# Kernel optimization log

Measured on AMD Instinct MI355X. Metric: run time of the kernel, lower is better.

Reference implementation:

```python
import jax, jax.numpy as jnp
import numpy as np

TOP_K = 4
N_GROUP = 8
TOPK_GROUP = 4
SCALE = 1.0

B, S, H, I, E = 2, 1024, 1024, 512, 32
SHARED_I = I * 2  # n_shared_experts = 2


def setup_inputs() -> dict:
    key = jax.random.key(0)
    ks = jax.random.split(key, 9)
    return {
        "hidden_states": jax.random.normal(ks[0], (B, S, H), jnp.float32),
        "gate_w": jax.random.normal(ks[1], (E, H), jnp.float32) * 0.02,
        "gate_bias": jnp.zeros((E,), jnp.float32),
        "gate_proj": jax.random.normal(ks[2], (E, I, H), jnp.float32) * 0.02,
        "up_proj": jax.random.normal(ks[3], (E, I, H), jnp.float32) * 0.02,
        "down_proj": jax.random.normal(ks[4], (E, H, I), jnp.float32) * 0.02,
        "shared_gate_w": jax.random.normal(ks[5], (SHARED_I, H), jnp.float32) * 0.02,
        "shared_up_w": jax.random.normal(ks[6], (SHARED_I, H), jnp.float32) * 0.02,
        "shared_down_w": jax.random.normal(ks[7], (H, SHARED_I), jnp.float32) * 0.02,
    }


def reference(hidden_states, gate_w, gate_bias, gate_proj, up_proj, down_proj,
              shared_gate_w, shared_up_w, shared_down_w):
    b, s, h = hidden_states.shape
    e = gate_w.shape[0]
    x = hidden_states.reshape(-1, h)            # (T, H)
    t = x.shape[0]

    # ---- gating (DeepSeek-V3 grouped sigmoid routing) ----
    logits = x @ gate_w.T                       # (T, E)
    scores = jax.nn.sigmoid(logits)
    sfc = scores + gate_bias[None, :]           # scores_for_choice
    # per-group score = sum of top-2 experts in group
    group_scores = jax.lax.top_k(sfc.reshape(t, N_GROUP, -1), 2)[0].sum(-1)  # (T, G)
    _, gidx = jax.lax.top_k(group_scores, TOPK_GROUP)                        # (T, topk_group)
    gmask = jax.nn.one_hot(gidx, N_GROUP, dtype=sfc.dtype).sum(1)            # (T, G)
    smask = jnp.repeat(gmask, e // N_GROUP, axis=1)                          # (T, E)
    tmp = jnp.where(smask > 0, sfc, 0.0)
    _, topk_idx = jax.lax.top_k(tmp, TOP_K)                                  # (T, K)
    topk_w = jnp.take_along_axis(scores, topk_idx, axis=1)                   # (T, K)
    topk_w = topk_w / (topk_w.sum(-1, keepdims=True) + 1e-20)                # norm_topk_prob
    topk_w = topk_w * SCALE

    # ---- routed experts (dense combine-weight formulation) ----
    comb = jnp.zeros((t, e), x.dtype).at[jnp.arange(t)[:, None], topk_idx].add(topk_w)  # (T, E)
    g = jnp.einsum('th,eih->eti', x, gate_proj)   # (E, T, I)
    u = jnp.einsum('th,eih->eti', x, up_proj)     # (E, T, I)
    a = jax.nn.silu(g) * u
    a = a * comb.T[:, :, None]                    # scale before down-proj to skip zero experts
    out = jnp.einsum('eti,ehi->th', a, down_proj) # (T, H)

    # ---- shared experts ----
    sg = x @ shared_gate_w.T
    su = x @ shared_up_w.T
    out = out + (jax.nn.silu(sg) * su) @ shared_down_w.T

    return out.reshape(b, s, h)
```

## Files before the change

kernel.cpp:

```cpp
#include <hip/hip_runtime.h>
#include <hip/hip_bf16.h>
#include <cstdint>
#include <cstddef>

#define H_DIM 1024
#define I_DIM 512
#define E_NUM 32
#define SHARED_I_DIM 1024
#define TOPK 4
#define NGROUP 8
#define TOPKG 4
#define GT 8

typedef __attribute__((ext_vector_type(8))) short bf16x8;
typedef __attribute__((ext_vector_type(4))) float f32x4;
typedef __attribute__((ext_vector_type(8))) unsigned short u16x8;

__device__ inline unsigned short f2bf(float f) {
    __hip_bfloat16 h = __float2bfloat16(f);
    return *reinterpret_cast<unsigned short*>(&h);
}
__device__ inline float bf2f(unsigned short u) {
    union { unsigned int u; float f; } w;
    w.u = ((unsigned int)u) << 16;
    return w.f;
}

__device__ inline int laddr(int row, int chunk) {
    return row * 32 + ((chunk ^ ((row >> 1) & 3)) << 3);
}

__global__ void init_kernel(int* cnt) {
    if (threadIdx.x < 64) cnt[threadIdx.x] = 0;
}

__global__ void cvt_kernel(const float* __restrict__ src, unsigned short* __restrict__ dst, int n8) {
    int i = blockIdx.x * blockDim.x + threadIdx.x;
    if (i >= n8) return;
    float4 a = *(const float4*)(src + (size_t)i * 8);
    float4 b = *(const float4*)(src + (size_t)i * 8 + 4);
    u16x8 v;
    v[0] = f2bf(a.x); v[1] = f2bf(a.y); v[2] = f2bf(a.z); v[3] = f2bf(a.w);
    v[4] = f2bf(b.x); v[5] = f2bf(b.y); v[6] = f2bf(b.z); v[7] = f2bf(b.w);
    *(u16x8*)(dst + (size_t)i * 8) = v;
}

__global__ __launch_bounds__(256) void gate_kernel(const float* __restrict__ x,
                                                   const float* __restrict__ gw,
                                                   float* __restrict__ logits_out) {
    int tb = blockIdx.x;
    int tid = threadIdx.x;
    __shared__ float xs[GT][H_DIM];
    __shared__ float ps[8][GT][E_NUM];
    const float* xsrc = x + (size_t)tb * GT * H_DIM;
    for (int i = tid; i < GT * H_DIM / 4; i += 256)
        ((float4*)&xs[0][0])[i] = ((const float4*)xsrc)[i];
    __syncthreads();
    int e = tid & 31, part = tid >> 5;
    const float* wrow = gw + (size_t)e * H_DIM + part * 128;
    float acc[GT] = {};
    for (int c0 = 0; c0 < 128; c0 += 32) {
        float w[32];
#pragma unroll
        for (int c = 0; c < 32; c++) w[c] = wrow[c0 + c];
#pragma unroll
        for (int t = 0; t < GT; t++) {
#pragma unroll
            for (int c = 0; c < 32; c++)
                acc[t] += w[c] * xs[t][part * 128 + c0 + c];
        }
    }
#pragma unroll
    for (int t = 0; t < GT; t++) ps[part][t][e] = acc[t];
    __syncthreads();
    {
        int t = tid >> 5, ee = tid & 31;
        float s = 0.f;
#pragma unroll
        for (int p = 0; p < 8; p++) s += ps[p][t][ee];
        logits_out[((size_t)tb * GT + t) * E_NUM + ee] = s;
    }
}

__global__ void select_kernel(const float* __restrict__ logits, const float* __restrict__ gb,
                              int* __restrict__ topk_e, float* __restrict__ topk_w,
                              int* __restrict__ cnt, int T) {
    int t = blockIdx.x * blockDim.x + threadIdx.x;
    if (t >= T) return;
    float scores[E_NUM], sfc[E_NUM];
#pragma unroll
    for (int i = 0; i < E_NUM; i++) {
        float l = logits[(size_t)t * E_NUM + i];
        float s = 1.f / (1.f + expf(-l));
        scores[i] = s;
        sfc[i] = s + gb[i];
    }
    float gs[NGROUP];
#pragma unroll
    for (int g = 0; g < NGROUP; g++) {
        float m1 = -1e30f, m2 = -1e30f;
#pragma unroll
        for (int j = 0; j < 4; j++) {
            float v = sfc[g * 4 + j];
            if (v > m1) { m2 = m1; m1 = v; }
            else if (v > m2) { m2 = v; }
        }
        gs[g] = m1 + m2;
    }
    unsigned gmask = 0;
    for (int r = 0; r < TOPKG; r++) {
        int best = 0; float bv = -1e30f;
#pragma unroll
        for (int g = 0; g < NGROUP; g++)
            if (!((gmask >> g) & 1u) && gs[g] > bv) { bv = gs[g]; best = g; }
        gmask |= 1u << best;
    }
    unsigned cmask = 0;
    int eidx[TOPK]; float ew[TOPK]; float sum = 0.f;
    for (int r = 0; r < TOPK; r++) {
        int best = 0; float bv = -1e30f; float bsc = 0.f;
#pragma unroll
        for (int i = 0; i < E_NUM; i++) {
            float v = ((gmask >> (i >> 2)) & 1u) ? sfc[i] : 0.0f;
            if (!((cmask >> i) & 1u) && v > bv) { bv = v; best = i; bsc = scores[i]; }
        }
        cmask |= 1u << best;
        eidx[r] = best; ew[r] = bsc; sum += bsc;
    }
    float inv = 1.f / (sum + 1e-20f);
#pragma unroll
    for (int k = 0; k < TOPK; k++) {
        topk_e[t * TOPK + k] = eidx[k];
        topk_w[t * TOPK + k] = ew[k] * inv;
        atomicAdd(&cnt[eidx[k]], 1);
    }
}

__global__ void scan_kernel(const int* __restrict__ cnt, int* __restrict__ off) {
    if (threadIdx.x == 0) {
        int a = 0;
        for (int e = 0; e < E_NUM; e++) { off[e] = a; a += cnt[e]; }
        off[E_NUM] = a;
    }
}

__global__ void bin_kernel(const int* __restrict__ topk_e, const float* __restrict__ topk_w,
                           const int* __restrict__ off, int* __restrict__ cnt2,
                           int* __restrict__ slot_token, float* __restrict__ slot_w,
                           int* __restrict__ slot_of, int total) {
    int i = blockIdx.x * blockDim.x + threadIdx.x;
    if (i >= total) return;
    int e = topk_e[i];
    float w = topk_w[i];
    int pos = atomicAdd(&cnt2[e], 1);
    int slot = off[e] + pos;
    slot_token[slot] = i >> 2;
    slot_w[slot] = w;
    slot_of[i] = slot;
}

__global__ __launch_bounds__(256) void combine_kernel(const unsigned short* __restrict__ out_slot,
                                                      const int* __restrict__ slot_of,
                                                      float* __restrict__ out) {
    int t = blockIdx.x;
    int h = threadIdx.x * 4;
    int s0 = slot_of[t * TOPK + 0], s1 = slot_of[t * TOPK + 1];
    int s2 = slot_of[t * TOPK + 2], s3 = slot_of[t * TOPK + 3];
    ushort4 a = *(const ushort4*)(out_slot + (size_t)s0 * H_DIM + h);
    ushort4 b = *(const ushort4*)(out_slot + (size_t)s1 * H_DIM + h);
    ushort4 c = *(const ushort4*)(out_slot + (size_t)s2 * H_DIM + h);
    ushort4 d = *(const ushort4*)(out_slot + (size_t)s3 * H_DIM + h);
    float4 o = *(float4*)(out + (size_t)t * H_DIM + h);
    o.x += bf2f(a.x) + bf2f(b.x) + bf2f(c.x) + bf2f(d.x);
    o.y += bf2f(a.y) + bf2f(b.y) + bf2f(c.y) + bf2f(d.y);
    o.z += bf2f(a.z) + bf2f(b.z) + bf2f(c.z) + bf2f(d.z);
    o.w += bf2f(a.w) + bf2f(b.w) + bf2f(c.w) + bf2f(d.w);
    *(float4*)(out + (size_t)t * H_DIM + h) = o;
}

template <bool STAGE1>
__global__ __launch_bounds__(512, 2) void moe_gemm(
    const unsigned short* __restrict__ Axr, const unsigned short* __restrict__ Axs,
    const float* __restrict__ B1r_, const float* __restrict__ B2r_,
    const float* __restrict__ B1s_, const float* __restrict__ B2s_,
    void* __restrict__ Dr, void* __restrict__ Ds,
    const int* __restrict__ slot_token, const float* __restrict__ slot_w,
    const int* __restrict__ cnt, const int* __restrict__ off_arr, int T) {
    constexpr bool DUAL = STAGE1;
    int e = blockIdx.x, itile = blockIdx.y, mtile = blockIdx.z;
    bool sh = (e == E_NUM);
    int NI = STAGE1 ? (sh ? 16 : 8) : 16;
    if (itile >= NI) return;
    int count = sh ? T : cnt[e];
    int base = sh ? 0 : off_arr[e];
    if (mtile * 256 >= count) return;
    const int K = STAGE1 ? H_DIM : (sh ? SHARED_I_DIM : I_DIM);

    __shared__ __align__(16) unsigned short As[2][256 * 32];
    __shared__ __align__(16) unsigned short Bs1[2][64 * 32];
    __shared__ __align__(16) unsigned short Bs2[2][DUAL ? 64 * 32 : 8];

    int tid = threadIdx.x, lane = tid & 63, wid = tid >> 6;

    int as_row = tid >> 1, as_c0 = (tid & 1) * 2;
    int am = mtile * 256 + as_row;
    int amc = (am < count) ? am : 0;
    const unsigned short* Abase;
    size_t arow;
    if constexpr (STAGE1) {
        Abase = Axr;
        arow = sh ? (size_t)amc : (size_t)slot_token[base + amc];
    } else {
        Abase = sh ? Axs : Axr;
        arow = sh ? (size_t)amc : (size_t)(base + amc);
    }
    const unsigned short* Ga = Abase + arow * K + as_c0 * 8;

    int bs_row = tid >> 3;
    int brow = itile * 64 + bs_row;
    int bwr = laddr(bs_row, (tid & 7) >> 1) + (tid & 1) * 4;
    const float* Gb1;
    const float* Gb2 = nullptr;
    if constexpr (STAGE1) {
        Gb1 = (sh ? B1s_ : (B1r_ + (size_t)e * (I_DIM * H_DIM))) + (size_t)brow * K + (tid & 7) * 4;
        Gb2 = (sh ? B2s_ : (B2r_ + (size_t)e * (I_DIM * H_DIM))) + (size_t)brow * K + (tid & 7) * 4;
    } else {
        Gb1 = (sh ? B1s_ : (B1r_ + (size_t)e * (H_DIM * I_DIM))) + (size_t)brow * K + (tid & 7) * 4;
    }

    f32x4 acc1[4][2] = {};
    f32x4 acc2[DUAL ? 4 : 1][2] = {};

    int wrow = (wid >> 1) * 64, wcol = (wid & 1) * 32;
    int frow = lane & 15, fch = lane >> 4;

    u16x8 a00, a01, a10, a11;
    float4 b10, b20, b11, b21;

    auto loadS = [&](u16x8& a0, u16x8& a1, float4& b1v, float4& b2v, int ks) {
        int k0 = ks << 5;
        a0 = *(const u16x8*)(Ga + k0);
        a1 = *(const u16x8*)(Ga + k0 + 8);
        b1v = *(const float4*)(Gb1 + k0);
        if constexpr (DUAL) b2v = *(const float4*)(Gb2 + k0);
    };
    auto writeS = [&](int buf, u16x8 a0, u16x8 a1, float4 b1v, float4 b2v) {
        *(u16x8*)(&As[buf][laddr(as_row, as_c0)]) = a0;
        *(u16x8*)(&As[buf][laddr(as_row, as_c0 + 1)]) = a1;
        ushort4 s;
        s.x = f2bf(b1v.x); s.y = f2bf(b1v.y); s.z = f2bf(b1v.z); s.w = f2bf(b1v.w);
        *(ushort4*)(&Bs1[buf][bwr]) = s;
        if constexpr (DUAL) {
            ushort4 s2;
            s2.x = f2bf(b2v.x); s2.y = f2bf(b2v.y); s2.z = f2bf(b2v.z); s2.w = f2bf(b2v.w);
            *(ushort4*)(&Bs2[buf][bwr]) = s2;
        }
    };
    auto compute = [&](int buf) {
        bf16x8 af[4], b1[2], b2[DUAL ? 2 : 1];
#pragma unroll
        for (int nf = 0; nf < 2; nf++)
            b1[nf] = *(const bf16x8*)(&Bs1[buf][laddr(wcol + nf * 16 + frow, fch)]);
        if constexpr (DUAL) {
#pragma unroll
            for (int nf = 0; nf < 2; nf++)
                b2[nf] = *(const bf16x8*)(&Bs2[buf][laddr(wcol + nf * 16 + frow, fch)]);
        }
#pragma unroll
        for (int mf = 0; mf < 4; mf++)
            af[mf] = *(const bf16x8*)(&As[buf][laddr(wrow + mf * 16 + frow, fch)]);
#pragma unroll
        for (int mf = 0; mf < 4; mf++)
#pragma unroll
            for (int nf = 0; nf < 2; nf++) {
                acc1[mf][nf] = __builtin_amdgcn_mfma_f32_16x16x32_bf16(af[mf], b1[nf], acc1[mf][nf], 0, 0, 0);
                if constexpr (DUAL)
                    acc2[mf][nf] = __builtin_amdgcn_mfma_f32_16x16x32_bf16(af[mf], b2[nf], acc2[mf][nf], 0, 0, 0);
            }
    };

    const int NK = K >> 5;
    loadS(a00, a01, b10, b20, 0);
    loadS(a10, a11, b11, b21, 1);
    writeS(0, a00, a01, b10, b20);
    loadS(a00, a01, b10, b20, 2);
    __syncthreads();
    for (int it = 0; it < NK; it += 2) {
        writeS(1, a10, a11, b11, b21);
        if (it + 3 < NK) loadS(a10, a11, b11, b21, it + 3);
        compute(0);
        __syncthreads();
        if (it + 2 < NK) {
            writeS(0, a00, a01, b10, b20);
            if (it + 4 < NK) loadS(a00, a01, b10, b20, it + 4);
        }
        compute(1);
        if (it + 2 < NK) __syncthreads();
    }

#pragma unroll
    for (int mf = 0; mf < 4; mf++)
#pragma unroll
        for (int nf = 0; nf < 2; nf++)
#pragma unroll
            for (int j = 0; j < 4; j++) {
                int rloc = wrow + mf * 16 + (lane >> 4) * 4 + j;
                int mrow = mtile * 256 + rloc;
                int col = itile * 64 + wcol + nf * 16 + (lane & 15);
                if (mrow >= count) continue;
                if constexpr (STAGE1) {
                    float w = sh ? 1.0f : slot_w[base + mrow];
                    float g = acc1[mf][nf][j];
                    float a = (g / (1.f + __expf(-g))) * acc2[mf][nf][j] * w;
                    if (sh) ((unsigned short*)Ds)[(size_t)mrow * SHARED_I_DIM + col] = f2bf(a);
                    else    ((unsigned short*)Dr)[(size_t)(base + mrow) * I_DIM + col] = f2bf(a);
                } else {
                    if (sh) ((float*)Ds)[(size_t)mrow * H_DIM + col] = acc1[mf][nf][j];
                    else    ((unsigned short*)Dr)[(size_t)(base + mrow) * H_DIM + col] = f2bf(acc1[mf][nf][j]);
                }
            }
}

extern "C" void kernel_launch(void* const* d_in, const int* in_sizes, int n_in,
                              void* d_out, int out_size, void* d_ws, size_t ws_size,
                              hipStream_t stream) {
    const float* x = (const float*)d_in[0];
    const float* gw = (const float*)d_in[1];
    const float* gb = (const float*)d_in[2];
    const float* gate_proj = (const float*)d_in[3];
    const float* up_proj = (const float*)d_in[4];
    const float* down_proj = (const float*)d_in[5];
    const float* sgw = (const float*)d_in[6];
    const float* suw = (const float*)d_in[7];
    const float* sdw = (const float*)d_in[8];
    float* out = (float*)d_out;

    const int T = in_sizes[0] / H_DIM;
    const int total_slots = T * TOPK;

    char* ws = (char*)d_ws;
    int* cnt = (int*)ws;
    int* cnt2 = cnt + 32;
    int* off = cnt + 64;
    int* topk_e = cnt + 128;
    float* topk_w = (float*)(topk_e + total_slots);
    int* slot_token = (int*)(topk_w + total_slots);
    float* slot_w = (float*)(slot_token + total_slots);
    int* slot_of = (int*)(slot_w + total_slots);
    float* logits = (float*)(slot_of + total_slots);
    unsigned short* x_bf = (unsigned short*)(logits + (size_t)T * E_NUM);
    unsigned short* act_r = x_bf + (size_t)T * H_DIM;
    unsigned short* act_s = act_r + (size_t)(total_slots + 256) * I_DIM;
    unsigned short* out_slot = act_s + (size_t)T * SHARED_I_DIM;

    hipLaunchKernelGGL(init_kernel, dim3(1), dim3(64), 0, stream, cnt);
    hipLaunchKernelGGL(cvt_kernel, dim3((T * H_DIM / 8 + 255) / 256), dim3(256), 0, stream,
                       x, x_bf, T * H_DIM / 8);
    hipLaunchKernelGGL(gate_kernel, dim3(T / GT), dim3(256), 0, stream, x, gw, logits);
    hipLaunchKernelGGL(select_kernel, dim3((T + 255) / 256), dim3(256), 0, stream,
                       logits, gb, topk_e, topk_w, cnt, T);
    hipLaunchKernelGGL(scan_kernel, dim3(1), dim3(1), 0, stream, cnt, off);
    hipLaunchKernelGGL(bin_kernel, dim3((total_slots + 255) / 256), dim3(256), 0, stream,
                       topk_e, topk_w, off, cnt2, slot_token, slot_w, slot_of, total_slots);

    hipLaunchKernelGGL((moe_gemm<true>), dim3(E_NUM + 1, 16, 32), dim3(512), 0, stream,
                       x_bf, (const unsigned short*)nullptr,
                       gate_proj, up_proj, sgw, suw,
                       (void*)act_r, (void*)act_s,
                       slot_token, slot_w, cnt, off, T);

    hipLaunchKernelGGL((moe_gemm<false>), dim3(E_NUM + 1, 16, 32), dim3(512), 0, stream,
                       act_r, act_s,
                       down_proj, (const float*)nullptr, sdw, (const float*)nullptr,
                       (void*)out_slot, (void*)out,
                       slot_token, slot_w, cnt, off, T);

    hipLaunchKernelGGL(combine_kernel, dim3(T), dim3(256), 0, stream, out_slot, slot_of, out);
}
```

Before: 195.0 us.

## Halve MoE GEMM M-tile, widen weight loads, use LDS-only barriers

The MoE GEMM blocks drop from 512 to 256 threads with a 128-row M tile, and the grid z shrinks to match. This gives more, smaller blocks, aiming for better load balance across the uneven per-expert token counts and higher occupancy. Each thread now loads 8 fp32 weights per row chunk and writes 16-byte LDS stores. __syncthreads is replaced by an lgkmcnt-only wait plus s_barrier, so prefetched global loads can stay in flight across barriers. The trade-off is that weight tiles are reloaded and converted to bf16 for twice as many M tiles.

Result: slower. 207.5 us (+6.4%).

```diff
diff --git a/kernel.cpp b/kernel.cpp
--- a/kernel.cpp
+++ b/kernel.cpp
@@ -24,6 +24,11 @@
     union { unsigned int u; float f; } w;
     w.u = ((unsigned int)u) << 16;
     return w.f;
+}
+
+__device__ inline void bar_lds() {
+    asm volatile("s_waitcnt lgkmcnt(0)" ::: "memory");
+    __builtin_amdgcn_s_barrier();
 }
 
 __device__ inline int laddr(int row, int chunk) {
@@ -179,7 +184,7 @@
 }
 
 template <bool STAGE1>
-__global__ __launch_bounds__(512, 2) void moe_gemm(
+__global__ __launch_bounds__(256, 3) void moe_gemm(
     const unsigned short* __restrict__ Axr, const unsigned short* __restrict__ Axs,
     const float* __restrict__ B1r_, const float* __restrict__ B2r_,
     const float* __restrict__ B1s_, const float* __restrict__ B2s_,
@@ -193,17 +198,17 @@
     if (itile >= NI) return;
     int count = sh ? T : cnt[e];
     int base = sh ? 0 : off_arr[e];
-    if (mtile * 256 >= count) return;
+    if (mtile * 128 >= count) return;
     const int K = STAGE1 ? H_DIM : (sh ? SHARED_I_DIM : I_DIM);
 
-    __shared__ __align__(16) unsigned short As[2][256 * 32];
+    __shared__ __align__(16) unsigned short As[2][128 * 32];
     __shared__ __align__(16) unsigned short Bs1[2][64 * 32];
     __shared__ __align__(16) unsigned short Bs2[2][DUAL ? 64 * 32 : 8];
 
     int tid = threadIdx.x, lane = tid & 63, wid = tid >> 6;
 
     int as_row = tid >> 1, as_c0 = (tid & 1) * 2;
-    int am = mtile * 256 + as_row;
+    int am = mtile * 128 + as_row;
     int amc = (am < count) ? am : 0;
     const unsigned short* Abase;
     size_t arow;
@@ -216,16 +221,16 @@
     }
     const unsigned short* Ga = Abase + arow * K + as_c0 * 8;
 
-    int bs_row = tid >> 3;
+    int bs_row = tid >> 2, bs_ch = tid & 3;
     int brow = itile * 64 + bs_row;
-    int bwr = laddr(bs_row, (tid & 7) >> 1) + (tid & 1) * 4;
+    int bwr = laddr(bs_row, bs_ch);
     const float* Gb1;
     const float* Gb2 = nullptr;
     if constexpr (STAGE1) {
-        Gb1 = (sh ? B1s_ : (B1r_ + (size_t)e * (I_DIM * H_DIM))) + (size_t)brow * K + (tid & 7) * 4;
-        Gb2 = (sh ? B2s_ : (B2r_ + (size_t)e * (I_DIM * H_DIM))) + (size_t)brow * K + (tid & 7) * 4;
+        Gb1 = (sh ? B1s_ : (B1r_ + (size_t)e * (I_DIM * H_DIM))) + (size_t)brow * K + bs_ch * 8;
+        Gb2 = (sh ? B2s_ : (B2r_ + (size_t)e * (I_DIM * H_DIM))) + (size_t)brow * K + bs_ch * 8;
     } else {
-        Gb1 = (sh ? B1s_ : (B1r_ + (size_t)e * (H_DIM * I_DIM))) + (size_t)brow * K + (tid & 7) * 4;
+        Gb1 = (sh ? B1s_ : (B1r_ + (size_t)e * (H_DIM * I_DIM))) + (size_t)brow * K + bs_ch * 8;
     }
 
     f32x4 acc1[4][2] = {};
@@ -235,25 +240,34 @@
     int frow = lane & 15, fch = lane >> 4;
 
     u16x8 a00, a01, a10, a11;
-    float4 b10, b20, b11, b21;
-
-    auto loadS = [&](u16x8& a0, u16x8& a1, float4& b1v, float4& b2v, int ks) {
+    float4 b1lo0, b1hi0, b2lo0, b2hi0;
+    float4 b1lo1, b1hi1, b2lo1, b2hi1;
+
+    auto loadS = [&](u16x8& a0, u16x8& a1, float4& b1lo, float4& b1hi,
+                     float4& b2lo, float4& b2hi, int ks) {
         int k0 = ks << 5;
         a0 = *(const u16x8*)(Ga + k0);
         a1 = *(const u16x8*)(Ga + k0 + 8);
-        b1v = *(const float4*)(Gb1 + k0);
-        if constexpr (DUAL) b2v = *(const float4*)(Gb2 + k0);
+        b1lo = *(const float4*)(Gb1 + k0);
+        b1hi = *(const float4*)(Gb1 + k0 + 4);
+        if constexpr (DUAL) {
+            b2lo = *(const float4*)(Gb2 + k0);
+            b2hi = *(const float4*)(Gb2 + k0 + 4);
+        }
     };
-    auto writeS = [&](int buf, u16x8 a0, u16x8 a1, float4 b1v, float4 b2v) {
+    auto writeS = [&](int buf, u16x8 a0, u16x8 a1, float4 b1lo, float4 b1hi,
+                      float4 b2lo, float4 b2hi) {
         *(u16x8*)(&As[buf][laddr(as_row, as_c0)]) = a0;
         *(u16x8*)(&As[buf][laddr(as_row, as_c0 + 1)]) = a1;
-        ushort4 s;
-        s.x = f2bf(b1v.x); s.y = f2bf(b1v.y); s.z = f2bf(b1v.z); s.w = f2bf(b1v.w);
-        *(ushort4*)(&Bs1[buf][bwr]) = s;
+        u16x8 s;
+        s[0] = f2bf(b1lo.x); s[1] = f2bf(b1lo.y); s[2] = f2bf(b1lo.z); s[3] = f2bf(b1lo.w);
+        s[4] = f2bf(b1hi.x); s[5] = f2bf(b1hi.y); s[6] = f2bf(b1hi.z); s[7] = f2bf(b1hi.w);
+        *(u16x8*)(&Bs1[buf][bwr]) = s;
         if constexpr (DUAL) {
-            ushort4 s2;
-            s2.x = f2bf(b2v.x); s2.y = f2bf(b2v.y); s2.z = f2bf(b2v.z); s2.w = f2bf(b2v.w);
-            *(ushort4*)(&Bs2[buf][bwr]) = s2;
+            u16x8 s2;
+            s2[0] = f2bf(b2lo.x); s2[1] = f2bf(b2lo.y); s2[2] = f2bf(b2lo.z); s2[3] = f2bf(b2lo.w);
+            s2[4] = f2bf(b2hi.x); s2[5] = f2bf(b2hi.y); s2[6] = f2bf(b2hi.z); s2[7] = f2bf(b2hi.w);
+            *(u16x8*)(&Bs2[buf][bwr]) = s2;
         }
     };
     auto compute = [&](int buf) {
@@ -280,22 +294,22 @@
     };
 
     const int NK = K >> 5;
-    loadS(a00, a01, b10, b20, 0);
-    loadS(a10, a11, b11, b21, 1);
-    writeS(0, a00, a01, b10, b20);
-    loadS(a00, a01, b10, b20, 2);
-    __syncthreads();
+    loadS(a00, a01, b1lo0, b1hi0, b2lo0, b2hi0, 0);
+    loadS(a10, a11, b1lo1, b1hi1, b2lo1, b2hi1, 1);
+    writeS(0, a00, a01, b1lo0, b1hi0, b2lo0, b2hi0);
+    loadS(a00, a01, b1lo0, b1hi0, b2lo0, b2hi0, 2);
+    bar_lds();
     for (int it = 0; it < NK; it += 2) {
-        writeS(1, a10, a11, b11, b21);
-        if (it + 3 < NK) loadS(a10, a11, b11, b21, it + 3);
+        writeS(1, a10, a11, b1lo1, b1hi1, b2lo1, b2hi1);
+        if (it + 3 < NK) loadS(a10, a11, b1lo1, b1hi1, b2lo1, b2hi1, it + 3);
         compute(0);
-        __syncthreads();
+        bar_lds();
         if (it + 2 < NK) {
-            writeS(0, a00, a01, b10, b20);
-            if (it + 4 < NK) loadS(a00, a01, b10, b20, it + 4);
+            writeS(0, a00, a01, b1lo0, b1hi0, b2lo0, b2hi0);
+            if (it + 4 < NK) loadS(a00, a01, b1lo0, b1hi0, b2lo0, b2hi0, it + 4);
         }
         compute(1);
-        if (it + 2 < NK) __syncthreads();
+        if (it + 2 < NK) bar_lds();
     }
 
 #pragma unroll
@@ -305,7 +319,7 @@
 #pragma unroll
             for (int j = 0; j < 4; j++) {
                 int rloc = wrow + mf * 16 + (lane >> 4) * 4 + j;
-                int mrow = mtile * 256 + rloc;
+                int mrow = mtile * 128 + rloc;
                 int col = itile * 64 + wcol + nf * 16 + (lane & 15);
                 if (mrow >= count) continue;
                 if constexpr (STAGE1) {
@@ -350,7 +364,7 @@
     float* logits = (float*)(slot_of + total_slots);
     unsigned short* x_bf = (unsigned short*)(logits + (size_t)T * E_NUM);
     unsigned short* act_r = x_bf + (size_t)T * H_DIM;
-    unsigned short* act_s = act_r + (size_t)(total_slots + 256) * I_DIM;
+    unsigned short* act_s = act_r + (size_t)(total_slots + 128) * I_DIM;
     unsigned short* out_slot = act_s + (size_t)T * SHARED_I_DIM;
 
     hipLaunchKernelGGL(init_kernel, dim3(1), dim3(64), 0, stream, cnt);
@@ -363,13 +377,13 @@
     hipLaunchKernelGGL(bin_kernel, dim3((total_slots + 255) / 256), dim3(256), 0, stream,
                        topk_e, topk_w, off, cnt2, slot_token, slot_w, slot_of, total_slots);
 
-    hipLaunchKernelGGL((moe_gemm<true>), dim3(E_NUM + 1, 16, 32), dim3(512), 0, stream,
+    hipLaunchKernelGGL((moe_gemm<true>), dim3(E_NUM + 1, 16, 16), dim3(256), 0, stream,
                        x_bf, (const unsigned short*)nullptr,
                        gate_proj, up_proj, sgw, suw,
                        (void*)act_r, (void*)act_s,
                        slot_token, slot_w, cnt, off, T);
 
-    hipLaunchKernelGGL((moe_gemm<false>), dim3(E_NUM + 1, 16, 32), dim3(512), 0, stream,
+    hipLaunchKernelGGL((moe_gemm<false>), dim3(E_NUM + 1, 16, 16), dim3(256), 0, stream,
                        act_r, act_s,
                        down_proj, (const float*)nullptr, sdw, (const float*)nullptr,
                        (void*)out_slot, (void*)out,
```

## Restructure MoE GEMMs as weight-stationary panels held in LDS

Applied to the files above, without the earlier changes.

Replaces the double-buffered tiled MoE GEMMs with weight-stationary kernels. Each block converts one narrow panel of expert weights (full K) to bf16 into LDS once, then its waves stream token rows directly from global memory. The goal is to read and convert each fp32 weight element only once instead of once per M tile, and to drop the per-k-step syncs. In exchange, A operands come straight from global memory with no LDS reuse, the N tiles are narrow (16 columns in stage 1), and per-expert work is serialised over only 4 waves per block, which may hurt load balance.

After: 313.8 us. 1.61x slower.

```diff
diff --git a/kernel.cpp b/kernel.cpp
--- a/kernel.cpp
+++ b/kernel.cpp
@@ -24,10 +24,6 @@
     union { unsigned int u; float f; } w;
     w.u = ((unsigned int)u) << 16;
     return w.f;
-}
-
-__device__ inline int laddr(int row, int chunk) {
-    return row * 32 + ((chunk ^ ((row >> 1) & 3)) << 3);
 }
 
 __global__ void init_kernel(int* cnt) {
@@ -178,147 +174,196 @@
     *(float4*)(out + (size_t)t * H_DIM + h) = o;
 }
 
-template <bool STAGE1>
-__global__ __launch_bounds__(512, 2) void moe_gemm(
-    const unsigned short* __restrict__ Axr, const unsigned short* __restrict__ Axs,
-    const float* __restrict__ B1r_, const float* __restrict__ B2r_,
-    const float* __restrict__ B1s_, const float* __restrict__ B2s_,
-    void* __restrict__ Dr, void* __restrict__ Ds,
+template <int NR, int KK>
+__device__ inline void ws_fill(const float* __restrict__ src, unsigned short* __restrict__ lds,
+                               int tid) {
+    constexpr int KK4 = KK / 4;
+    constexpr int TOT = NR * KK4;
+#pragma unroll
+    for (int i = 0; i < TOT / 256; ++i) {
+        int idx = i * 256 + tid;
+        int row = idx / KK4;
+        int col4 = idx - row * KK4;
+        float4 v = *(const float4*)(src + (size_t)idx * 4);
+        ushort4 s;
+        s.x = f2bf(v.x); s.y = f2bf(v.y); s.z = f2bf(v.z); s.w = f2bf(v.w);
+        int chunk = col4 >> 1, sub = (col4 & 1) << 2;
+        *(ushort4*)(lds + row * KK + ((chunk ^ (row & 7)) << 3) + sub) = s;
+    }
+}
+
+template <int NF, int NK, bool DUAL, int LROW>
+__device__ inline void ws_core(const unsigned short* __restrict__ A0,
+                               const unsigned short* __restrict__ A1,
+                               const unsigned short* __restrict__ A2,
+                               const unsigned short* __restrict__ A3,
+                               const unsigned short* __restrict__ LB1,
+                               const unsigned short* __restrict__ LB2,
+                               int lane, f32x4 (&acc1)[4][NF], f32x4 (&acc2)[4][NF]) {
+    int frow = lane & 15, fk = lane >> 4;
+#pragma unroll 4
+    for (int ks = 0; ks < NK; ++ks) {
+        int k0 = ks * 32;
+        bf16x8 af[4];
+        af[0] = *(const bf16x8*)(A0 + k0);
+        af[1] = *(const bf16x8*)(A1 + k0);
+        af[2] = *(const bf16x8*)(A2 + k0);
+        af[3] = *(const bf16x8*)(A3 + k0);
+        bf16x8 b1[NF], b2[DUAL ? NF : 1];
+#pragma unroll
+        for (int nf = 0; nf < NF; nf++) {
+            int r = nf * 16 + frow;
+            int addr = r * LROW + ((((k0 >> 3) + fk) ^ (r & 7)) << 3);
+            b1[nf] = *(const bf16x8*)(LB1 + addr);
+            if constexpr (DUAL) b2[nf] = *(const bf16x8*)(LB2 + addr);
+        }
+#pragma unroll
+        for (int m = 0; m < 4; m++)
+#pragma unroll
+            for (int nf = 0; nf < NF; nf++) {
+                acc1[m][nf] = __builtin_amdgcn_mfma_f32_16x16x32_bf16(af[m], b1[nf], acc1[m][nf], 0, 0, 0);
+                if constexpr (DUAL)
+                    acc2[m][nf] = __builtin_amdgcn_mfma_f32_16x16x32_bf16(af[m], b2[nf], acc2[m][nf], 0, 0, 0);
+            }
+    }
+}
+
+__global__ __launch_bounds__(256, 2) void moe_ws1(
+    const unsigned short* __restrict__ x_bf,
+    const float* __restrict__ gate_proj, const float* __restrict__ up_proj,
+    const float* __restrict__ sgw, const float* __restrict__ suw,
+    unsigned short* __restrict__ act_r, unsigned short* __restrict__ act_s,
     const int* __restrict__ slot_token, const float* __restrict__ slot_w,
-    const int* __restrict__ cnt, const int* __restrict__ off_arr, int T) {
-    constexpr bool DUAL = STAGE1;
-    int e = blockIdx.x, itile = blockIdx.y, mtile = blockIdx.z;
+    const int* __restrict__ cnt, const int* __restrict__ off_arr) {
+    int e = blockIdx.x, panel = blockIdx.y, mz = blockIdx.z;
     bool sh = (e == E_NUM);
-    int NI = STAGE1 ? (sh ? 16 : 8) : 16;
-    if (itile >= NI) return;
-    int count = sh ? T : cnt[e];
-    int base = sh ? 0 : off_arr[e];
-    if (mtile * 256 >= count) return;
-    const int K = STAGE1 ? H_DIM : (sh ? SHARED_I_DIM : I_DIM);
-
-    __shared__ __align__(16) unsigned short As[2][256 * 32];
-    __shared__ __align__(16) unsigned short Bs1[2][64 * 32];
-    __shared__ __align__(16) unsigned short Bs2[2][DUAL ? 64 * 32 : 8];
-
+    __shared__ __align__(16) unsigned short LB1[16 * 1024];
+    __shared__ __align__(16) unsigned short LB2[16 * 1024];
     int tid = threadIdx.x, lane = tid & 63, wid = tid >> 6;
-
-    int as_row = tid >> 1, as_c0 = (tid & 1) * 2;
-    int am = mtile * 256 + as_row;
-    int amc = (am < count) ? am : 0;
-    const unsigned short* Abase;
-    size_t arow;
-    if constexpr (STAGE1) {
-        Abase = Axr;
-        arow = sh ? (size_t)amc : (size_t)slot_token[base + amc];
+    int frow = lane & 15, fk = lane >> 4;
+
+    if (!sh) {
+        if (panel >= 32 || mz > 0) return;
+        int count = cnt[e], base = off_arr[e];
+        if (count == 0) return;
+        ws_fill<16, 1024>(gate_proj + ((size_t)e * I_DIM + panel * 16) * H_DIM, LB1, tid);
+        ws_fill<16, 1024>(up_proj + ((size_t)e * I_DIM + panel * 16) * H_DIM, LB2, tid);
+        __syncthreads();
+        int G = (count + 63) >> 6;
+        for (int g = wid; g < G; g += 4) {
+            const unsigned short* Ap[4];
+#pragma unroll
+            for (int m = 0; m < 4; m++) {
+                int am = g * 64 + m * 16 + frow;
+                int ams = (am < count) ? am : 0;
+                int tok = slot_token[base + ams];
+                Ap[m] = x_bf + (size_t)tok * H_DIM + fk * 8;
+            }
+            f32x4 acc1[4][1] = {};
+            f32x4 acc2[4][1] = {};
+            ws_core<1, 32, true, 1024>(Ap[0], Ap[1], Ap[2], Ap[3], LB1, LB2, lane, acc1, acc2);
+#pragma unroll
+            for (int m = 0; m < 4; m++)
+#pragma unroll
+                for (int j = 0; j < 4; j++) {
+                    int mrow = g * 64 + m * 16 + fk * 4 + j;
+                    if (mrow >= count) continue;
+                    float w = slot_w[base + mrow];
+                    float gg = acc1[m][0][j];
+                    float a = (gg / (1.f + __expf(-gg))) * acc2[m][0][j] * w;
+                    act_r[(size_t)(base + mrow) * I_DIM + panel * 16 + frow] = f2bf(a);
+                }
+        }
     } else {
-        Abase = sh ? Axs : Axr;
-        arow = sh ? (size_t)amc : (size_t)(base + amc);
-    }
-    const unsigned short* Ga = Abase + arow * K + as_c0 * 8;
-
-    int bs_row = tid >> 3;
-    int brow = itile * 64 + bs_row;
-    int bwr = laddr(bs_row, (tid & 7) >> 1) + (tid & 1) * 4;
-    const float* Gb1;
-    const float* Gb2 = nullptr;
-    if constexpr (STAGE1) {
-        Gb1 = (sh ? B1s_ : (B1r_ + (size_t)e * (I_DIM * H_DIM))) + (size_t)brow * K + (tid & 7) * 4;
-        Gb2 = (sh ? B2s_ : (B2r_ + (size_t)e * (I_DIM * H_DIM))) + (size_t)brow * K + (tid & 7) * 4;
+        ws_fill<16, 1024>(sgw + (size_t)panel * 16 * H_DIM, LB1, tid);
+        ws_fill<16, 1024>(suw + (size_t)panel * 16 * H_DIM, LB2, tid);
+        __syncthreads();
+        for (int g = wid; g < 8; g += 4) {
+            int rb = mz * 512 + g * 64;
+            const unsigned short* Ap[4];
+#pragma unroll
+            for (int m = 0; m < 4; m++)
+                Ap[m] = x_bf + (size_t)(rb + m * 16 + frow) * H_DIM + fk * 8;
+            f32x4 acc1[4][1] = {};
+            f32x4 acc2[4][1] = {};
+            ws_core<1, 32, true, 1024>(Ap[0], Ap[1], Ap[2], Ap[3], LB1, LB2, lane, acc1, acc2);
+#pragma unroll
+            for (int m = 0; m < 4; m++)
+#pragma unroll
+                for (int j = 0; j < 4; j++) {
+                    int t = rb + m * 16 + fk * 4 + j;
+                    float gg = acc1[m][0][j];
+                    float a = (gg / (1.f + __expf(-gg))) * acc2[m][0][j];
+                    act_s[(size_t)t * SHARED_I_DIM + panel * 16 + frow] = f2bf(a);
+                }
+        }
+    }
+}
+
+__global__ __launch_bounds__(256, 2) void moe_ws2(
+    const unsigned short* __restrict__ act_r, const unsigned short* __restrict__ act_s,
+    const float* __restrict__ down_proj, const float* __restrict__ sdw,
+    unsigned short* __restrict__ out_slot, float* __restrict__ out,
+    const int* __restrict__ cnt, const int* __restrict__ off_arr) {
+    int e = blockIdx.x, panel = blockIdx.y, mz = blockIdx.z;
+    bool sh = (e == E_NUM);
+    __shared__ __align__(16) unsigned short LB[32 * 1024];
+    int tid = threadIdx.x, lane = tid & 63, wid = tid >> 6;
+    int frow = lane & 15, fk = lane >> 4;
+
+    if (!sh) {
+        if (panel >= 16 || mz > 0) return;
+        int count = cnt[e], base = off_arr[e];
+        if (count == 0) return;
+        ws_fill<64, 512>(down_proj + ((size_t)e * H_DIM + panel * 64) * I_DIM, LB, tid);
+        __syncthreads();
+        int G = (count + 63) >> 6;
+        for (int g = wid; g < G; g += 4) {
+            const unsigned short* Ap[4];
+#pragma unroll
+            for (int m = 0; m < 4; m++) {
+                int am = g * 64 + m * 16 + frow;
+                int ams = (am < count) ? am : 0;
+                Ap[m] = act_r + (size_t)(base + ams) * I_DIM + fk * 8;
+            }
+            f32x4 acc1[4][4] = {};
+            f32x4 acc2[4][4] = {};
+            ws_core<4, 16, false, 512>(Ap[0], Ap[1], Ap[2], Ap[3], LB, LB, lane, acc1, acc2);
+#pragma unroll
+            for (int m = 0; m < 4; m++)
+#pragma unroll
+                for (int nf = 0; nf < 4; nf++)
+#pragma unroll
+                    for (int j = 0; j < 4; j++) {
+                        int mrow = g * 64 + m * 16 + fk * 4 + j;
+                        if (mrow >= count) continue;
+                        out_slot[(size_t)(base + mrow) * H_DIM + panel * 64 + nf * 16 + frow] =
+                            f2bf(acc1[m][nf][j]);
+                    }
+        }
     } else {
-        Gb1 = (sh ? B1s_ : (B1r_ + (size_t)e * (H_DIM * I_DIM))) + (size_t)brow * K + (tid & 7) * 4;
-    }
-
-    f32x4 acc1[4][2] = {};
-    f32x4 acc2[DUAL ? 4 : 1][2] = {};
-
-    int wrow = (wid >> 1) * 64, wcol = (wid & 1) * 32;
-    int frow = lane & 15, fch = lane >> 4;
-
-    u16x8 a00, a01, a10, a11;
-    float4 b10, b20, b11, b21;
-
-    auto loadS = [&](u16x8& a0, u16x8& a1, float4& b1v, float4& b2v, int ks) {
-        int k0 = ks << 5;
-        a0 = *(const u16x8*)(Ga + k0);
-        a1 = *(const u16x8*)(Ga + k0 + 8);
-        b1v = *(const float4*)(Gb1 + k0);
-        if constexpr (DUAL) b2v = *(const float4*)(Gb2 + k0);
-    };
-    auto writeS = [&](int buf, u16x8 a0, u16x8 a1, float4 b1v, float4 b2v) {
-        *(u16x8*)(&As[buf][laddr(as_row, as_c0)]) = a0;
-        *(u16x8*)(&As[buf][laddr(as_row, as_c0 + 1)]) = a1;
-        ushort4 s;
-        s.x = f2bf(b1v.x); s.y = f2bf(b1v.y); s.z = f2bf(b1v.z); s.w = f2bf(b1v.w);
-        *(ushort4*)(&Bs1[buf][bwr]) = s;
-        if constexpr (DUAL) {
-            ushort4 s2;
-            s2.x = f2bf(b2v.x); s2.y = f2bf(b2v.y); s2.z = f2bf(b2v.z); s2.w = f2bf(b2v.w);
-            *(ushort4*)(&Bs2[buf][bwr]) = s2;
-        }
-    };
-    auto compute = [&](int buf) {
-        bf16x8 af[4], b1[2], b2[DUAL ? 2 : 1];
-#pragma unroll
-        for (int nf = 0; nf < 2; nf++)
-            b1[nf] = *(const bf16x8*)(&Bs1[buf][laddr(wcol + nf * 16 + frow, fch)]);
-        if constexpr (DUAL) {
-#pragma unroll
-            for (int nf = 0; nf < 2; nf++)
-                b2[nf] = *(const bf16x8*)(&Bs2[buf][laddr(wcol + nf * 16 + frow, fch)]);
-        }
-#pragma unroll
-        for (int mf = 0; mf < 4; mf++)
-            af[mf] = *(const bf16x8*)(&As[buf][laddr(wrow + mf * 16 + frow, fch)]);
-#pragma unroll
-        for (int mf = 0; mf < 4; mf++)
-#pragma unroll
-            for (int nf = 0; nf < 2; nf++) {
-                acc1[mf][nf] = __builtin_amdgcn_mfma_f32_16x16x32_bf16(af[mf], b1[nf], acc1[mf][nf], 0, 0, 0);
-                if constexpr (DUAL)
-                    acc2[mf][nf] = __builtin_amdgcn_mfma_f32_16x16x32_bf16(af[mf], b2[nf], acc2[mf][nf], 0, 0, 0);
-            }
-    };
-
-    const int NK = K >> 5;
-    loadS(a00, a01, b10, b20, 0);
-    loadS(a10, a11, b11, b21, 1);
-    writeS(0, a00, a01, b10, b20);
-    loadS(a00, a01, b10, b20, 2);
-    __syncthreads();
-    for (int it = 0; it < NK; it += 2) {
-        writeS(1, a10, a11, b11, b21);
-        if (it + 3 < NK) loadS(a10, a11, b11, b21, it + 3);
-        compute(0);
+        ws_fill<32, 1024>(sdw + (size_t)panel * 32 * SHARED_I_DIM, LB, tid);
         __syncthreads();
-        if (it + 2 < NK) {
-            writeS(0, a00, a01, b10, b20);
-            if (it + 4 < NK) loadS(a00, a01, b10, b20, it + 4);
-        }
-        compute(1);
-        if (it + 2 < NK) __syncthreads();
-    }
-
-#pragma unroll
-    for (int mf = 0; mf < 4; mf++)
-#pragma unroll
-        for (int nf = 0; nf < 2; nf++)
-#pragma unroll
-            for (int j = 0; j < 4; j++) {
-                int rloc = wrow + mf * 16 + (lane >> 4) * 4 + j;
-                int mrow = mtile * 256 + rloc;
-                int col = itile * 64 + wcol + nf * 16 + (lane & 15);
-                if (mrow >= count) continue;
-                if constexpr (STAGE1) {
-                    float w = sh ? 1.0f : slot_w[base + mrow];
-                    float g = acc1[mf][nf][j];
-                    float a = (g / (1.f + __expf(-g))) * acc2[mf][nf][j] * w;
-                    if (sh) ((unsigned short*)Ds)[(size_t)mrow * SHARED_I_DIM + col] = f2bf(a);
-                    else    ((unsigned short*)Dr)[(size_t)(base + mrow) * I_DIM + col] = f2bf(a);
-                } else {
-                    if (sh) ((float*)Ds)[(size_t)mrow * H_DIM + col] = acc1[mf][nf][j];
-                    else    ((unsigned short*)Dr)[(size_t)(base + mrow) * H_DIM + col] = f2bf(acc1[mf][nf][j]);
-                }
-            }
+        for (int g = wid; g < 8; g += 4) {
+            int rb = mz * 512 + g * 64;
+            const unsigned short* Ap[4];
+#pragma unroll
+            for (int m = 0; m < 4; m++)
+                Ap[m] = act_s + (size_t)(rb + m * 16 + frow) * SHARED_I_DIM + fk * 8;
+            f32x4 acc1[4][2] = {};
+            f32x4 acc2[4][2] = {};
+            ws_core<2, 32, false, 1024>(Ap[0], Ap[1], Ap[2], Ap[3], LB, LB, lane, acc1, acc2);
+#pragma unroll
+            for (int m = 0; m < 4; m++)
+#pragma unroll
+                for (int nf = 0; nf < 2; nf++)
+#pragma unroll
+                    for (int j = 0; j < 4; j++) {
+                        int t = rb + m * 16 + fk * 4 + j;
+                        out[(size_t)t * H_DIM + panel * 32 + nf * 16 + frow] = acc1[m][nf][j];
+                    }
+        }
+    }
 }
 
 extern "C" void kernel_launch(void* const* d_in, const int* in_sizes, int n_in,
@@ -350,7 +395,7 @@
     float* logits = (float*)(slot_of + total_slots);
     unsigned short* x_bf = (unsigned short*)(logits + (size_t)T * E_NUM);
     unsigned short* act_r = x_bf + (size_t)T * H_DIM;
-    unsigned short* act_s = act_r + (size_t)(total_slots + 256) * I_DIM;
+    unsigned short* act_s = act_r + (size_t)(total_slots + 128) * I_DIM;
     unsigned short* out_slot = act_s + (size_t)T * SHARED_I_DIM;
 
     hipLaunchKernelGGL(init_kernel, dim3(1), dim3(64), 0, stream, cnt);
@@ -363,17 +408,13 @@
     hipLaunchKernelGGL(bin_kernel, dim3((total_slots + 255) / 256), dim3(256), 0, stream,
                        topk_e, topk_w, off, cnt2, slot_token, slot_w, slot_of, total_slots);
 
-    hipLaunchKernelGGL((moe_gemm<true>), dim3(E_NUM + 1, 16, 32), dim3(512), 0, stream,
-                       x_bf, (const unsigned short*)nullptr,
-                       gate_proj, up_proj, sgw, suw,
-                       (void*)act_r, (void*)act_s,
-                       slot_token, slot_w, cnt, off, T);
-
-    hipLaunchKernelGGL((moe_gemm<false>), dim3(E_NUM + 1, 16, 32), dim3(512), 0, stream,
-                       act_r, act_s,
-                       down_proj, (const float*)nullptr, sdw, (const float*)nullptr,
-                       (void*)out_slot, (void*)out,
-                       slot_token, slot_w, cnt, off, T);
+    hipLaunchKernelGGL(moe_ws1, dim3(E_NUM + 1, 64, 4), dim3(256), 0, stream,
+                       x_bf, gate_proj, up_proj, sgw, suw,
+                       act_r, act_s, slot_token, slot_w, cnt, off);
+
+    hipLaunchKernelGGL(moe_ws2, dim3(E_NUM + 1, 32, 4), dim3(256), 0, stream,
+                       act_r, act_s, down_proj, sdw,
+                       out_slot, out, cnt, off);
 
     hipLaunchKernelGGL(combine_kernel, dim3(T), dim3(256), 0, stream, out_slot, slot_of, out);
 }
```

## Narrow GEMM N-tile to 32, loop M-tiles persistently, split B loads by half-block

Applied to the files above, without the earlier changes.

Shrinks the MoE GEMM tile from 256x64 to 256x32 and doubles the itile grid. Blocks now loop over M-tiles with a stride of 8 instead of launching one block per M-tile. Half the threads load gate weights and the other half load up weights, and the barrier is replaced with an explicit lgkmcnt wait plus s_barrier. The shared expert is split across z into 256-row chunks. The goal is better load balance and occupancy across uneven expert counts and less idle grid overhead, at the cost of lower per-block arithmetic intensity and more re-reading of A.

After: 232.5 us. 19.2% more time.

```diff
diff --git a/kernel.cpp b/kernel.cpp
--- a/kernel.cpp
+++ b/kernel.cpp
@@ -24,6 +24,11 @@
     union { unsigned int u; float f; } w;
     w.u = ((unsigned int)u) << 16;
     return w.f;
+}
+
+__device__ inline void bar_lds() {
+    asm volatile("s_waitcnt lgkmcnt(0)" ::: "memory");
+    __builtin_amdgcn_s_barrier();
 }
 
 __device__ inline int laddr(int row, int chunk) {
@@ -187,138 +192,163 @@
     const int* __restrict__ slot_token, const float* __restrict__ slot_w,
     const int* __restrict__ cnt, const int* __restrict__ off_arr, int T) {
     constexpr bool DUAL = STAGE1;
-    int e = blockIdx.x, itile = blockIdx.y, mtile = blockIdx.z;
+    int e = blockIdx.x, itile = blockIdx.y, zz = blockIdx.z;
     bool sh = (e == E_NUM);
-    int NI = STAGE1 ? (sh ? 16 : 8) : 16;
+    int NI = STAGE1 ? (sh ? 32 : 16) : 32;
     if (itile >= NI) return;
-    int count = sh ? T : cnt[e];
-    int base = sh ? 0 : off_arr[e];
-    if (mtile * 256 >= count) return;
+    int count, base;
+    if (sh) { count = 256; base = zz * 256; }
+    else {
+        count = cnt[e]; base = off_arr[e];
+        if (zz * 256 >= count) return;
+    }
     const int K = STAGE1 ? H_DIM : (sh ? SHARED_I_DIM : I_DIM);
 
     __shared__ __align__(16) unsigned short As[2][256 * 32];
-    __shared__ __align__(16) unsigned short Bs1[2][64 * 32];
-    __shared__ __align__(16) unsigned short Bs2[2][DUAL ? 64 * 32 : 8];
+    __shared__ __align__(16) unsigned short Bs1[2][32 * 32];
+    __shared__ __align__(16) unsigned short Bs2[2][DUAL ? 32 * 32 : 8];
 
     int tid = threadIdx.x, lane = tid & 63, wid = tid >> 6;
+    int frow = lane & 15, fch = lane >> 4;
+    int wrow = wid * 32;
+
+    int bhalf = tid >> 8, bt = tid & 255;
+    int b_row = bt >> 3, b_q = bt & 7;
+    int brow = itile * 32 + b_row;
+    const float* Gb = nullptr;
+    bool doB;
+    if constexpr (STAGE1) {
+        doB = true;
+        const float* Bb = sh ? (bhalf ? B2s_ : B1s_)
+                             : ((bhalf ? B2r_ : B1r_) + (size_t)e * I_DIM * H_DIM);
+        Gb = Bb + (size_t)brow * K + b_q * 4;
+    } else {
+        doB = (bhalf == 0);
+        if (doB) {
+            const float* Bb = sh ? B1s_ : (B1r_ + (size_t)e * H_DIM * I_DIM);
+            Gb = Bb + (size_t)brow * K + b_q * 4;
+        }
+    }
+    int bwr = laddr(b_row, b_q >> 1) + (b_q & 1) * 4;
 
     int as_row = tid >> 1, as_c0 = (tid & 1) * 2;
-    int am = mtile * 256 + as_row;
-    int amc = (am < count) ? am : 0;
-    const unsigned short* Abase;
-    size_t arow;
-    if constexpr (STAGE1) {
-        Abase = Axr;
-        arow = sh ? (size_t)amc : (size_t)slot_token[base + amc];
-    } else {
-        Abase = sh ? Axs : Axr;
-        arow = sh ? (size_t)amc : (size_t)(base + amc);
-    }
-    const unsigned short* Ga = Abase + arow * K + as_c0 * 8;
-
-    int bs_row = tid >> 3;
-    int brow = itile * 64 + bs_row;
-    int bwr = laddr(bs_row, (tid & 7) >> 1) + (tid & 1) * 4;
-    const float* Gb1;
-    const float* Gb2 = nullptr;
-    if constexpr (STAGE1) {
-        Gb1 = (sh ? B1s_ : (B1r_ + (size_t)e * (I_DIM * H_DIM))) + (size_t)brow * K + (tid & 7) * 4;
-        Gb2 = (sh ? B2s_ : (B2r_ + (size_t)e * (I_DIM * H_DIM))) + (size_t)brow * K + (tid & 7) * 4;
-    } else {
-        Gb1 = (sh ? B1s_ : (B1r_ + (size_t)e * (H_DIM * I_DIM))) + (size_t)brow * K + (tid & 7) * 4;
-    }
-
-    f32x4 acc1[4][2] = {};
-    f32x4 acc2[DUAL ? 4 : 1][2] = {};
-
-    int wrow = (wid >> 1) * 64, wcol = (wid & 1) * 32;
-    int frow = lane & 15, fch = lane >> 4;
-
-    u16x8 a00, a01, a10, a11;
-    float4 b10, b20, b11, b21;
-
-    auto loadS = [&](u16x8& a0, u16x8& a1, float4& b1v, float4& b2v, int ks) {
-        int k0 = ks << 5;
-        a0 = *(const u16x8*)(Ga + k0);
-        a1 = *(const u16x8*)(Ga + k0 + 8);
-        b1v = *(const float4*)(Gb1 + k0);
-        if constexpr (DUAL) b2v = *(const float4*)(Gb2 + k0);
-    };
-    auto writeS = [&](int buf, u16x8 a0, u16x8 a1, float4 b1v, float4 b2v) {
-        *(u16x8*)(&As[buf][laddr(as_row, as_c0)]) = a0;
-        *(u16x8*)(&As[buf][laddr(as_row, as_c0 + 1)]) = a1;
-        ushort4 s;
-        s.x = f2bf(b1v.x); s.y = f2bf(b1v.y); s.z = f2bf(b1v.z); s.w = f2bf(b1v.w);
-        *(ushort4*)(&Bs1[buf][bwr]) = s;
-        if constexpr (DUAL) {
-            ushort4 s2;
-            s2.x = f2bf(b2v.x); s2.y = f2bf(b2v.y); s2.z = f2bf(b2v.z); s2.w = f2bf(b2v.w);
-            *(ushort4*)(&Bs2[buf][bwr]) = s2;
-        }
-    };
-    auto compute = [&](int buf) {
-        bf16x8 af[4], b1[2], b2[DUAL ? 2 : 1];
-#pragma unroll
-        for (int nf = 0; nf < 2; nf++)
-            b1[nf] = *(const bf16x8*)(&Bs1[buf][laddr(wcol + nf * 16 + frow, fch)]);
-        if constexpr (DUAL) {
+
+    const int NK = K >> 5;
+
+    for (int mt = zz; ; mt += 8) {
+        if (!sh && mt * 256 >= count) break;
+
+        int am = (sh ? 0 : mt * 256) + as_row;
+        int ams = (am < count) ? am : (count - 1);
+        const unsigned short* Ga;
+        if constexpr (STAGE1) {
+            size_t tok = sh ? (size_t)(base + ams) : (size_t)slot_token[base + ams];
+            Ga = Axr + tok * (size_t)H_DIM + as_c0 * 8;
+        } else {
+            Ga = sh ? (Axs + (size_t)(base + ams) * K + as_c0 * 8)
+                    : (Axr + (size_t)(base + ams) * K + as_c0 * 8);
+        }
+
+        f32x4 acc1[2][2] = {};
+        f32x4 acc2[DUAL ? 2 : 1][2] = {};
+
+        u16x8 a00, a01, a10, a11;
+        float4 bv0, bv1;
+
+        auto loadS = [&](u16x8& a0, u16x8& a1, float4& bv, int ks) {
+            int k0 = ks << 5;
+            a0 = *(const u16x8*)(Ga + k0);
+            a1 = *(const u16x8*)(Ga + k0 + 8);
+            if (doB) bv = *(const float4*)(Gb + k0);
+        };
+        auto writeS = [&](int buf, u16x8 a0, u16x8 a1, float4 bv) {
+            *(u16x8*)(&As[buf][laddr(as_row, as_c0)]) = a0;
+            *(u16x8*)(&As[buf][laddr(as_row, as_c0 + 1)]) = a1;
+            if (doB) {
+                ushort4 s;
+                s.x = f2bf(bv.x); s.y = f2bf(bv.y); s.z = f2bf(bv.z); s.w = f2bf(bv.w);
+                unsigned short* d = (DUAL && bhalf) ? &Bs2[buf][0] : &Bs1[buf][0];
+                *(ushort4*)(&d[bwr]) = s;
+            }
+        };
+        auto compute = [&](int buf) {
+            bf16x8 af[2], b1[2], b2[DUAL ? 2 : 1];
 #pragma unroll
             for (int nf = 0; nf < 2; nf++)
-                b2[nf] = *(const bf16x8*)(&Bs2[buf][laddr(wcol + nf * 16 + frow, fch)]);
-        }
-#pragma unroll
-        for (int mf = 0; mf < 4; mf++)
-            af[mf] = *(const bf16x8*)(&As[buf][laddr(wrow + mf * 16 + frow, fch)]);
-#pragma unroll
-        for (int mf = 0; mf < 4; mf++)
-#pragma unroll
-            for (int nf = 0; nf < 2; nf++) {
-                acc1[mf][nf] = __builtin_amdgcn_mfma_f32_16x16x32_bf16(af[mf], b1[nf], acc1[mf][nf], 0, 0, 0);
-                if constexpr (DUAL)
-                    acc2[mf][nf] = __builtin_amdgcn_mfma_f32_16x16x32_bf16(af[mf], b2[nf], acc2[mf][nf], 0, 0, 0);
+                b1[nf] = *(const bf16x8*)(&Bs1[buf][laddr(nf * 16 + frow, fch)]);
+            if constexpr (DUAL) {
+#pragma unroll
+                for (int nf = 0; nf < 2; nf++)
+                    b2[nf] = *(const bf16x8*)(&Bs2[buf][laddr(nf * 16 + frow, fch)]);
             }
-    };
-
-    const int NK = K >> 5;
-    loadS(a00, a01, b10, b20, 0);
-    loadS(a10, a11, b11, b21, 1);
-    writeS(0, a00, a01, b10, b20);
-    loadS(a00, a01, b10, b20, 2);
-    __syncthreads();
-    for (int it = 0; it < NK; it += 2) {
-        writeS(1, a10, a11, b11, b21);
-        if (it + 3 < NK) loadS(a10, a11, b11, b21, it + 3);
-        compute(0);
-        __syncthreads();
-        if (it + 2 < NK) {
-            writeS(0, a00, a01, b10, b20);
-            if (it + 4 < NK) loadS(a00, a01, b10, b20, it + 4);
-        }
-        compute(1);
-        if (it + 2 < NK) __syncthreads();
-    }
-
-#pragma unroll
-    for (int mf = 0; mf < 4; mf++)
-#pragma unroll
-        for (int nf = 0; nf < 2; nf++)
-#pragma unroll
-            for (int j = 0; j < 4; j++) {
-                int rloc = wrow + mf * 16 + (lane >> 4) * 4 + j;
-                int mrow = mtile * 256 + rloc;
-                int col = itile * 64 + wcol + nf * 16 + (lane & 15);
-                if (mrow >= count) continue;
-                if constexpr (STAGE1) {
-                    float w = sh ? 1.0f : slot_w[base + mrow];
-                    float g = acc1[mf][nf][j];
-                    float a = (g / (1.f + __expf(-g))) * acc2[mf][nf][j] * w;
-                    if (sh) ((unsigned short*)Ds)[(size_t)mrow * SHARED_I_DIM + col] = f2bf(a);
-                    else    ((unsigned short*)Dr)[(size_t)(base + mrow) * I_DIM + col] = f2bf(a);
-                } else {
-                    if (sh) ((float*)Ds)[(size_t)mrow * H_DIM + col] = acc1[mf][nf][j];
-                    else    ((unsigned short*)Dr)[(size_t)(base + mrow) * H_DIM + col] = f2bf(acc1[mf][nf][j]);
+#pragma unroll
+            for (int mf = 0; mf < 2; mf++)
+                af[mf] = *(const bf16x8*)(&As[buf][laddr(wrow + mf * 16 + frow, fch)]);
+#pragma unroll
+            for (int mf = 0; mf < 2; mf++)
+#pragma unroll
+                for (int nf = 0; nf < 2; nf++) {
+                    acc1[mf][nf] = __builtin_amdgcn_mfma_f32_16x16x32_bf16(af[mf], b1[nf], acc1[mf][nf], 0, 0, 0);
+                    if constexpr (DUAL)
+                        acc2[mf][nf] = __builtin_amdgcn_mfma_f32_16x16x32_bf16(af[mf], b2[nf], acc2[mf][nf], 0, 0, 0);
                 }
+        };
+
+        loadS(a00, a01, bv0, 0);
+        loadS(a10, a11, bv1, 1);
+        writeS(0, a00, a01, bv0);
+        loadS(a00, a01, bv0, 2);
+        bar_lds();
+        for (int it = 0; it < NK; it += 2) {
+            writeS(1, a10, a11, bv1);
+            if (it + 3 < NK) loadS(a10, a11, bv1, it + 3);
+            compute(0);
+            bar_lds();
+            if (it + 2 < NK) {
+                writeS(0, a00, a01, bv0);
+                if (it + 4 < NK) loadS(a00, a01, bv0, it + 4);
             }
+            compute(1);
+            if (it + 2 < NK) bar_lds();
+        }
+
+#pragma unroll
+        for (int mf = 0; mf < 2; mf++)
+#pragma unroll
+            for (int nf = 0; nf < 2; nf++)
+#pragma unroll
+                for (int j = 0; j < 4; j++) {
+                    int rloc = wrow + mf * 16 + fch * 4 + j;
+                    int col = itile * 32 + nf * 16 + frow;
+                    if constexpr (STAGE1) {
+                        if (sh) {
+                            int t = base + rloc;
+                            float g = acc1[mf][nf][j];
+                            float a = (g / (1.f + __expf(-g))) * acc2[mf][nf][j];
+                            ((unsigned short*)Ds)[(size_t)t * SHARED_I_DIM + col] = f2bf(a);
+                        } else {
+                            int mrow = mt * 256 + rloc;
+                            if (mrow >= count) continue;
+                            float w = slot_w[base + mrow];
+                            float g = acc1[mf][nf][j];
+                            float a = (g / (1.f + __expf(-g))) * acc2[mf][nf][j] * w;
+                            ((unsigned short*)Dr)[(size_t)(base + mrow) * I_DIM + col] = f2bf(a);
+                        }
+                    } else {
+                        if (sh) {
+                            int t = base + rloc;
+                            ((float*)Ds)[(size_t)t * H_DIM + col] = acc1[mf][nf][j];
+                        } else {
+                            int mrow = mt * 256 + rloc;
+                            if (mrow >= count) continue;
+                            ((unsigned short*)Dr)[(size_t)(base + mrow) * H_DIM + col] = f2bf(acc1[mf][nf][j]);
+                        }
+                    }
+                }
+
+        if (sh) break;
+        bar_lds();
+    }
 }
 
 extern "C" void kernel_launch(void* const* d_in, const int* in_sizes, int n_in,
@@ -363,13 +393,13 @@
     hipLaunchKernelGGL(bin_kernel, dim3((total_slots + 255) / 256), dim3(256), 0, stream,
                        topk_e, topk_w, off, cnt2, slot_token, slot_w, slot_of, total_slots);
 
-    hipLaunchKernelGGL((moe_gemm<true>), dim3(E_NUM + 1, 16, 32), dim3(512), 0, stream,
+    hipLaunchKernelGGL((moe_gemm<true>), dim3(E_NUM + 1, 32, 8), dim3(512), 0, stream,
                        x_bf, (const unsigned short*)nullptr,
                        gate_proj, up_proj, sgw, suw,
                        (void*)act_r, (void*)act_s,
                        slot_token, slot_w, cnt, off, T);
 
-    hipLaunchKernelGGL((moe_gemm<false>), dim3(E_NUM + 1, 16, 32), dim3(512), 0, stream,
+    hipLaunchKernelGGL((moe_gemm<false>), dim3(E_NUM + 1, 32, 8), dim3(512), 0, stream,
                        act_r, act_s,
                        down_proj, (const float*)nullptr, sdw, (const float*)nullptr,
                        (void*)out_slot, (void*)out,
```
